# Optimization experiments

Hardware: AMD Instinct MI355X
Metric: run time of the kernel (lower is better)

## Reference

```python
import jax, jax.numpy as jnp
import numpy as np

D_MODEL = 1024
D_STATE = 64
B = 8
L = 8192
REAL_INIT = -0.5
SCALING = 1.0


def _hippo_frequencies(d_state):
    # eigenvalues of (Hippo - Hippo.T)/2, largest imag part first
    N = 2 * d_state
    i = np.arange(N, dtype=np.float64)
    x = 2 * i + 1
    Hippo = np.tril(np.sqrt(np.outer(x, x)), k=-1)
    Skew = (Hippo - Hippo.T) / 2
    evals = np.linalg.eigvals(Skew)
    order = np.argsort(-evals.imag)
    return evals[order][:d_state].imag.astype(np.float32)


def setup_inputs() -> dict:
    key = jax.random.key(0)
    k1, k2, k3, k4 = jax.random.split(key, 4)
    frequencies = jnp.asarray(_hippo_frequencies(D_STATE) * SCALING)
    decays = jnp.full((D_STATE,), np.float32(np.log(abs(REAL_INIT) * SCALING + 1e-10)))
    return {
        "input": jax.random.normal(k1, (B, L, D_MODEL), dtype=jnp.float32),
        "initial_state": jax.random.normal(k2, (B, D_STATE), dtype=jnp.float32),
        "in_projection": jax.random.normal(k3, (D_MODEL, D_STATE), dtype=jnp.float32),
        "out_projection": jax.random.normal(k4, (D_STATE, D_MODEL), dtype=jnp.float32),
        "frequencies": frequencies,
        "decays": decays,
    }


def reference(input, initial_state, in_projection, out_projection, frequencies, decays):
    Bsz, Lseq, H = input.shape
    # project into state space: [B, L, N]
    u = jnp.einsum("blh,hn->bln", input, in_projection)
    # prepend initial state: [B, L+1, N]
    u = jnp.concatenate((initial_state[:, None, :].astype(u.dtype), u), axis=1)
    kernel_len = Lseq + 1
    fft_len = 2 * kernel_len - 1
    # diagonal SSM kernel: exp(t * (-exp(decay) + i*freq)), t = 0..L  -> [kernel_len, N]
    lam = (-jnp.exp(decays) + 1j * frequencies).astype(jnp.complex64)  # [N]
    t = jnp.arange(kernel_len, dtype=jnp.float32)[:, None]  # [kernel_len, 1]
    kernel = jnp.exp(t * lam[None, :])
    # FFT convolution along sequence axis
    u_f = jnp.fft.fft(u, n=fft_len, axis=-2)
    k_f = jnp.fft.fft(kernel, n=fft_len, axis=-2)
    conv = jnp.fft.ifft(u_f * k_f[None, :, :], axis=-2)[:, 1:Lseq + 1, :]
    final_state = conv[:, -1:, :]  # [B, 1, N] complex
    output = jnp.einsum("bln,nh->blh", conv.real, out_projection)
    return output, final_state
```

## Files before the change

kernel.cpp:

```cpp
#include <hip/hip_runtime.h>
#include <math.h>

#define Bz   8
#define Lz   8192
#define Hz   1024
#define Nz   64
#define BLz  (Bz * Lz)

typedef __attribute__((ext_vector_type(8))) short bf16x8;
typedef __attribute__((ext_vector_type(4))) float f32x4;

__device__ inline unsigned int bfpack2(float a, float b) {
    unsigned int ua = __float_as_uint(a) + 0x8000u;
    unsigned int ub = __float_as_uint(b) + 0x8000u;
    return (ua >> 16) | (ub & 0xFFFF0000u);
}
__device__ inline unsigned short bf1(float a) {
    return (unsigned short)((__float_as_uint(a) + 0x8000u) >> 16);
}

__global__ __launch_bounds__(256) void prep_kernel(
    const float* __restrict__ Win, const float* __restrict__ Wout,
    unsigned short* __restrict__ WinT, unsigned short* __restrict__ WoutT)
{
    int i = blockIdx.x * 256 + threadIdx.x;
    if (i < 65536) {
        int n = i >> 10, k = i & 1023;
        WinT[i] = bf1(Win[k * Nz + n]);
    } else {
        int j = i - 65536;
        int h = j >> 6, n = j & 63;
        WoutT[j] = bf1(Wout[n * Hz + h]);
    }
}

__global__ __launch_bounds__(256) void gemm_in_kernel(
    const float* __restrict__ inp, const unsigned short* __restrict__ WinT,
    float* __restrict__ u)
{
    __shared__ unsigned short sA[128][72];
    __shared__ unsigned short sB[64][72];

    const int t    = threadIdx.x;
    const int wid  = t >> 6;
    const int lane = t & 63;
    const int nl   = lane & 15;
    const int q    = lane >> 4;
    const size_t rowBase = (size_t)blockIdx.x * 128;

    f32x4 acc[2][4];
#pragma unroll
    for (int m = 0; m < 2; ++m)
#pragma unroll
        for (int nt = 0; nt < 4; ++nt) acc[m][nt] = (f32x4){0.f, 0.f, 0.f, 0.f};

    for (int kc = 0; kc < Hz; kc += 64) {
        __syncthreads();
#pragma unroll
        for (int j = 0; j < 4; ++j) {
            int f = j * 256 + t;
            int r = f >> 3, c = f & 7;
            const float* p = inp + (rowBase + r) * Hz + kc + c * 8;
            float4 v0 = *reinterpret_cast<const float4*>(p);
            float4 v1 = *reinterpret_cast<const float4*>(p + 4);
            uint4 d;
            d.x = bfpack2(v0.x, v0.y);
            d.y = bfpack2(v0.z, v0.w);
            d.z = bfpack2(v1.x, v1.y);
            d.w = bfpack2(v1.z, v1.w);
            *reinterpret_cast<uint4*>(&sA[r][c * 8]) = d;
        }
#pragma unroll
        for (int j = 0; j < 2; ++j) {
            int f = j * 256 + t;
            int r = f >> 3, c = f & 7;
            uint4 w = *reinterpret_cast<const uint4*>(WinT + (size_t)r * Hz + kc + c * 8);
            *reinterpret_cast<uint4*>(&sB[r][c * 8]) = w;
        }
        __syncthreads();

#pragma unroll
        for (int ks = 0; ks < 2; ++ks) {
            bf16x8 a0 = *reinterpret_cast<bf16x8*>(&sA[wid * 32 + nl][ks * 32 + q * 8]);
            bf16x8 a1 = *reinterpret_cast<bf16x8*>(&sA[wid * 32 + 16 + nl][ks * 32 + q * 8]);
#pragma unroll
            for (int nt = 0; nt < 4; ++nt) {
                bf16x8 b = *reinterpret_cast<bf16x8*>(&sB[nt * 16 + nl][ks * 32 + q * 8]);
                acc[0][nt] = __builtin_amdgcn_mfma_f32_16x16x32_bf16(a0, b, acc[0][nt], 0, 0, 0);
                acc[1][nt] = __builtin_amdgcn_mfma_f32_16x16x32_bf16(a1, b, acc[1][nt], 0, 0, 0);
            }
        }
    }

    const int bI = (int)(rowBase >> 13);
    const int l0 = ((int)rowBase & (Lz - 1)) + wid * 32 + q * 4;
#pragma unroll
    for (int m = 0; m < 2; ++m)
#pragma unroll
        for (int nt = 0; nt < 4; ++nt) {
            const int nn = nt * 16 + nl;
            *reinterpret_cast<f32x4*>(
                u + (((size_t)(bI * Nz + nn)) << 13) + (l0 + m * 16)) = acc[m][nt];
        }
}

#define CHUNK 512
#define WARM  192
#define GSTEP 64

#define SSTEP(UV, IDX)                                              \
    {                                                               \
        float nr_ = fmaf(ar, xr, fmaf(-ai, xi, (UV)));              \
        float ni_ = fmaf(ar, xi, ai * xr);                          \
        xr = nr_; xi = ni_;                                         \
        if (emit_) cp_[(size_t)(IDX) * Nz] = bf1(xr);               \
    }

#define DO_GROUP(BUF, G)                                            \
    {                                                               \
        const int g_ = (G);                                         \
        const bool emit_ = (g_ >= emitG);                           \
        const bool pf_ = (g_ + 2 < nG);                             \
        unsigned short* cp_ = cb + (size_t)(g_ * GSTEP) * Nz;       \
        const float4* np_ = up + (g_ + 2) * (GSTEP / 4);            \
        _Pragma("unroll")                                           \
        for (int k = 0; k < 16; ++k) {                              \
            float4 v_ = BUF[k];                                     \
            if (pf_) BUF[k] = np_[k];                               \
            SSTEP(v_.x, k * 4 + 0)                                  \
            SSTEP(v_.y, k * 4 + 1)                                  \
            SSTEP(v_.z, k * 4 + 2)                                  \
            SSTEP(v_.w, k * 4 + 3)                                  \
        }                                                           \
    }

__global__ __launch_bounds__(64) void scan_kernel(
    const float* __restrict__ ut, const float* __restrict__ init,
    const float* __restrict__ freq, const float* __restrict__ dec,
    unsigned short* __restrict__ convb, float* __restrict__ fs, int fs_mode)
{
    const int n = threadIdx.x;
    const int b = blockIdx.x;
    const int c = blockIdx.y;

    const float mag = expf(-expf(dec[n]));
    const float fr  = freq[n];
    const float ar  = mag * cosf(fr);
    const float ai  = mag * sinf(fr);

    const int s0    = (c == 0) ? 0 : (c * CHUNK - WARM);
    const int nG    = (c == 0) ? (CHUNK / GSTEP) : ((CHUNK + WARM) / GSTEP);
    const int emitG = (c == 0) ? 0 : (WARM / GSTEP);

    const float4* up = reinterpret_cast<const float4*>(
                           ut + (((size_t)(b * Nz + n)) << 13)) + (s0 >> 2);
    unsigned short* cb = convb + ((size_t)b * Lz + s0) * Nz + n;

    float xr = (c == 0) ? init[b * Nz + n] : 0.f;
    float xi = 0.f;

    float4 bufA[16], bufB[16];
#pragma unroll
    for (int k = 0; k < 16; ++k) bufA[k] = up[k];
#pragma unroll
    for (int k = 0; k < 16; ++k) bufB[k] = up[16 + k];

    const int nG2 = nG & ~1;
    for (int g = 0; g < nG2; g += 2) {
        DO_GROUP(bufA, g)
        DO_GROUP(bufB, g + 1)
    }
    if (nG & 1) { DO_GROUP(bufA, nG - 1) }

    if (c == (Lz / CHUNK) - 1 && fs_mode) {
        if (fs_mode == 2) {
            fs[(b * Nz + n) * 2 + 0] = xr;
            fs[(b * Nz + n) * 2 + 1] = xi;
        } else {
            fs[b * Nz + n] = xr;
        }
    }
}

__global__ __launch_bounds__(512) void gemm_out_kernel(
    const unsigned short* __restrict__ convb,
    const unsigned short* __restrict__ WoutT,
    float* __restrict__ out)
{
    __shared__ unsigned short sW[256][72];

    const int t    = threadIdx.x;
    const int wid  = t >> 6;
    const int lane = t & 63;
    const int nl   = lane & 15;
    const int q    = lane >> 4;
    const int hBase = blockIdx.x * 256;
    const size_t rowBase = (size_t)blockIdx.y * 128 + wid * 16;

#pragma unroll
    for (int j = 0; j < 4; ++j) {
        int f = j * 512 + t;
        int r = f >> 3, c = f & 7;
        uint4 v = *reinterpret_cast<const uint4*>(WoutT + (size_t)(hBase + r) * Nz + c * 8);
        *reinterpret_cast<uint4*>(&sW[r][c * 8]) = v;
    }
    __syncthreads();

    const unsigned short* ap = convb + (rowBase + nl) * Nz;
    bf16x8 a0 = *reinterpret_cast<const bf16x8*>(ap + q * 8);
    bf16x8 a1 = *reinterpret_cast<const bf16x8*>(ap + 32 + q * 8);

    const f32x4 zero = (f32x4){0.f, 0.f, 0.f, 0.f};
#pragma unroll
    for (int ht = 0; ht < 16; ++ht) {
        bf16x8 b0 = *reinterpret_cast<bf16x8*>(&sW[ht * 16 + nl][q * 8]);
        bf16x8 b1 = *reinterpret_cast<bf16x8*>(&sW[ht * 16 + nl][32 + q * 8]);
        f32x4 acc = __builtin_amdgcn_mfma_f32_16x16x32_bf16(a0, b0, zero, 0, 0, 0);
        acc = __builtin_amdgcn_mfma_f32_16x16x32_bf16(a1, b1, acc, 0, 0, 0);
#pragma unroll
        for (int reg = 0; reg < 4; ++reg)
            out[(rowBase + q * 4 + reg) * Hz + hBase + ht * 16 + nl] = acc[reg];
    }
}

extern "C" void kernel_launch(void* const* d_in, const int* in_sizes, int n_in,
                              void* d_out, int out_size, void* d_ws, size_t ws_size,
                              hipStream_t stream)
{
    const float* inp  = (const float*)d_in[0];
    const float* init = (const float*)d_in[1];
    const float* Win  = (const float*)d_in[2];
    const float* Wout = (const float*)d_in[3];
    const float* freq = (const float*)d_in[4];
    const float* dec  = (const float*)d_in[5];
    float* out = (float*)d_out;

    char* ws = (char*)d_ws;
    float*          u     = (float*)ws;
    unsigned short* convb = (unsigned short*)(ws + (size_t)BLz * Nz * 4);
    unsigned short* WinT  = (unsigned short*)(ws + (size_t)BLz * Nz * 6);
    unsigned short* WoutT = WinT + (size_t)Nz * Hz;

    const int extra   = out_size - BLz * Hz;
    const int fs_mode = (extra >= 2 * Bz * Nz) ? 2 : (extra >= Bz * Nz ? 1 : 0);
    float* fs = out + (size_t)BLz * Hz;

    hipLaunchKernelGGL(prep_kernel, dim3(512), dim3(256), 0, stream,
                       Win, Wout, WinT, WoutT);
    hipLaunchKernelGGL(gemm_in_kernel, dim3(BLz / 128), dim3(256), 0, stream,
                       inp, WinT, u);
    hipLaunchKernelGGL(scan_kernel, dim3(Bz, Lz / CHUNK), dim3(64), 0, stream,
                       u, init, freq, dec, convb, fs, fs_mode);
    hipLaunchKernelGGL(gemm_out_kernel, dim3(Hz / 256, BLz / 128), dim3(512), 0, stream,
                       convb, WoutT, out);
}
```

Baseline: 512.9 us.

## Load GEMM operands straight to registers with double buffering; transpose output MFMA for vector stores

The input-projection GEMM drops its shared-memory staging and syncthreads. Each single-wave block now loads fp32 activations and bf16 weights directly into registers, converting them in flight, with a two-stage register double buffer across K chunks. The output GEMM swaps the MFMA operand order so each lane holds contiguous output columns and writes them as float4 vector stores instead of scalar strided stores. The trade-off is higher register pressure and redundant weight loads from global/L2 in every block, in exchange for less LDS traffic and barrier overhead.

```diff
diff --git a/kernel.cpp b/kernel.cpp
--- a/kernel.cpp
+++ b/kernel.cpp
@@ -17,6 +17,14 @@
 }
 __device__ inline unsigned short bf1(float a) {
     return (unsigned short)((__float_as_uint(a) + 0x8000u) >> 16);
+}
+__device__ inline bf16x8 packa(float4 v0, float4 v1) {
+    union { uint4 u; bf16x8 h; } cv;
+    cv.u.x = bfpack2(v0.x, v0.y);
+    cv.u.y = bfpack2(v0.z, v0.w);
+    cv.u.z = bfpack2(v1.x, v1.y);
+    cv.u.w = bfpack2(v1.z, v1.w);
+    return cv.h;
 }
 
 __global__ __launch_bounds__(256) void prep_kernel(
@@ -34,19 +42,62 @@
     }
 }
 
-__global__ __launch_bounds__(256) void gemm_in_kernel(
+#define LOADKC(AB, BB, OFF)                                                  \
+    if ((OFF) < Hz) {                                                        \
+        const float* ap0_ = a0p + (OFF);                                     \
+        const float* ap1_ = a1p + (OFF);                                     \
+        AB[0] = *reinterpret_cast<const float4*>(ap0_);                      \
+        AB[1] = *reinterpret_cast<const float4*>(ap0_ + 4);                  \
+        AB[2] = *reinterpret_cast<const float4*>(ap0_ + 32);                 \
+        AB[3] = *reinterpret_cast<const float4*>(ap0_ + 36);                 \
+        AB[4] = *reinterpret_cast<const float4*>(ap1_);                      \
+        AB[5] = *reinterpret_cast<const float4*>(ap1_ + 4);                  \
+        AB[6] = *reinterpret_cast<const float4*>(ap1_ + 32);                 \
+        AB[7] = *reinterpret_cast<const float4*>(ap1_ + 36);                 \
+        BB[0] = *reinterpret_cast<const bf16x8*>(b0p + (OFF));               \
+        BB[1] = *reinterpret_cast<const bf16x8*>(b0p + (OFF) + 32);          \
+        BB[2] = *reinterpret_cast<const bf16x8*>(b1p + (OFF));               \
+        BB[3] = *reinterpret_cast<const bf16x8*>(b1p + (OFF) + 32);          \
+        BB[4] = *reinterpret_cast<const bf16x8*>(b2p + (OFF));               \
+        BB[5] = *reinterpret_cast<const bf16x8*>(b2p + (OFF) + 32);          \
+        BB[6] = *reinterpret_cast<const bf16x8*>(b3p + (OFF));               \
+        BB[7] = *reinterpret_cast<const bf16x8*>(b3p + (OFF) + 32);          \
+    }
+
+#define CONSKC(AB, BB)                                                       \
+    {                                                                        \
+        bf16x8 a00 = packa(AB[0], AB[1]);                                    \
+        bf16x8 a01 = packa(AB[2], AB[3]);                                    \
+        bf16x8 a10 = packa(AB[4], AB[5]);                                    \
+        bf16x8 a11 = packa(AB[6], AB[7]);                                    \
+        _Pragma("unroll")                                                    \
+        for (int nt = 0; nt < 4; ++nt) {                                     \
+            acc[0][nt] = __builtin_amdgcn_mfma_f32_16x16x32_bf16(            \
+                a00, BB[nt * 2 + 0], acc[0][nt], 0, 0, 0);                   \
+            acc[0][nt] = __builtin_amdgcn_mfma_f32_16x16x32_bf16(            \
+                a01, BB[nt * 2 + 1], acc[0][nt], 0, 0, 0);                   \
+            acc[1][nt] = __builtin_amdgcn_mfma_f32_16x16x32_bf16(            \
+                a10, BB[nt * 2 + 0], acc[1][nt], 0, 0, 0);                   \
+            acc[1][nt] = __builtin_amdgcn_mfma_f32_16x16x32_bf16(            \
+                a11, BB[nt * 2 + 1], acc[1][nt], 0, 0, 0);                   \
+        }                                                                    \
+    }
+
+__global__ __launch_bounds__(64) void gemm_in_kernel(
     const float* __restrict__ inp, const unsigned short* __restrict__ WinT,
     float* __restrict__ u)
 {
-    __shared__ unsigned short sA[128][72];
-    __shared__ unsigned short sB[64][72];
-
-    const int t    = threadIdx.x;
-    const int wid  = t >> 6;
-    const int lane = t & 63;
+    const int lane = threadIdx.x;
     const int nl   = lane & 15;
     const int q    = lane >> 4;
-    const size_t rowBase = (size_t)blockIdx.x * 128;
+    const size_t rowBase = (size_t)blockIdx.x * 32;
+
+    const float* a0p = inp + (rowBase + nl) * Hz + q * 8;
+    const float* a1p = inp + (rowBase + 16 + nl) * Hz + q * 8;
+    const unsigned short* b0p = WinT + (size_t)(0 * 16 + nl) * Hz + q * 8;
+    const unsigned short* b1p = WinT + (size_t)(1 * 16 + nl) * Hz + q * 8;
+    const unsigned short* b2p = WinT + (size_t)(2 * 16 + nl) * Hz + q * 8;
+    const unsigned short* b3p = WinT + (size_t)(3 * 16 + nl) * Hz + q * 8;
 
     f32x4 acc[2][4];
 #pragma unroll
@@ -54,46 +105,21 @@
 #pragma unroll
         for (int nt = 0; nt < 4; ++nt) acc[m][nt] = (f32x4){0.f, 0.f, 0.f, 0.f};
 
-    for (int kc = 0; kc < Hz; kc += 64) {
-        __syncthreads();
-#pragma unroll
-        for (int j = 0; j < 4; ++j) {
-            int f = j * 256 + t;
-            int r = f >> 3, c = f & 7;
-            const float* p = inp + (rowBase + r) * Hz + kc + c * 8;
-            float4 v0 = *reinterpret_cast<const float4*>(p);
-            float4 v1 = *reinterpret_cast<const float4*>(p + 4);
-            uint4 d;
-            d.x = bfpack2(v0.x, v0.y);
-            d.y = bfpack2(v0.z, v0.w);
-            d.z = bfpack2(v1.x, v1.y);
-            d.w = bfpack2(v1.z, v1.w);
-            *reinterpret_cast<uint4*>(&sA[r][c * 8]) = d;
-        }
-#pragma unroll
-        for (int j = 0; j < 2; ++j) {
-            int f = j * 256 + t;
-            int r = f >> 3, c = f & 7;
-            uint4 w = *reinterpret_cast<const uint4*>(WinT + (size_t)r * Hz + kc + c * 8);
-            *reinterpret_cast<uint4*>(&sB[r][c * 8]) = w;
-        }
-        __syncthreads();
-
-#pragma unroll
-        for (int ks = 0; ks < 2; ++ks) {
-            bf16x8 a0 = *reinterpret_cast<bf16x8*>(&sA[wid * 32 + nl][ks * 32 + q * 8]);
-            bf16x8 a1 = *reinterpret_cast<bf16x8*>(&sA[wid * 32 + 16 + nl][ks * 32 + q * 8]);
-#pragma unroll
-            for (int nt = 0; nt < 4; ++nt) {
-                bf16x8 b = *reinterpret_cast<bf16x8*>(&sB[nt * 16 + nl][ks * 32 + q * 8]);
-                acc[0][nt] = __builtin_amdgcn_mfma_f32_16x16x32_bf16(a0, b, acc[0][nt], 0, 0, 0);
-                acc[1][nt] = __builtin_amdgcn_mfma_f32_16x16x32_bf16(a1, b, acc[1][nt], 0, 0, 0);
-            }
-        }
+    float4 A0[8], A1[8];
+    bf16x8 B0[8], B1[8];
+    LOADKC(A0, B0, 0)
+    LOADKC(A1, B1, 64)
+
+#pragma unroll
+    for (int g = 0; g < 8; ++g) {
+        CONSKC(A0, B0)
+        LOADKC(A0, B0, g * 128 + 128)
+        CONSKC(A1, B1)
+        LOADKC(A1, B1, g * 128 + 192)
     }
 
     const int bI = (int)(rowBase >> 13);
-    const int l0 = ((int)rowBase & (Lz - 1)) + wid * 32 + q * 4;
+    const int l0 = ((int)rowBase & (Lz - 1)) + q * 4;
 #pragma unroll
     for (int m = 0; m < 2; ++m)
 #pragma unroll
@@ -195,7 +221,7 @@
     const int nl   = lane & 15;
     const int q    = lane >> 4;
     const int hBase = blockIdx.x * 256;
-    const size_t rowBase = (size_t)blockIdx.y * 128 + wid * 16;
+    const size_t blBase = (size_t)blockIdx.y * 128 + wid * 16;
 
 #pragma unroll
     for (int j = 0; j < 4; ++j) {
@@ -204,22 +230,21 @@
         uint4 v = *reinterpret_cast<const uint4*>(WoutT + (size_t)(hBase + r) * Nz + c * 8);
         *reinterpret_cast<uint4*>(&sW[r][c * 8]) = v;
     }
+
+    const unsigned short* bp = convb + (blBase + nl) * Nz + q * 8;
+    bf16x8 b0 = *reinterpret_cast<const bf16x8*>(bp);
+    bf16x8 b1 = *reinterpret_cast<const bf16x8*>(bp + 32);
     __syncthreads();
 
-    const unsigned short* ap = convb + (rowBase + nl) * Nz;
-    bf16x8 a0 = *reinterpret_cast<const bf16x8*>(ap + q * 8);
-    bf16x8 a1 = *reinterpret_cast<const bf16x8*>(ap + 32 + q * 8);
-
+    float* op = out + (blBase + nl) * Hz + hBase + q * 4;
     const f32x4 zero = (f32x4){0.f, 0.f, 0.f, 0.f};
 #pragma unroll
     for (int ht = 0; ht < 16; ++ht) {
-        bf16x8 b0 = *reinterpret_cast<bf16x8*>(&sW[ht * 16 + nl][q * 8]);
-        bf16x8 b1 = *reinterpret_cast<bf16x8*>(&sW[ht * 16 + nl][32 + q * 8]);
-        f32x4 acc = __builtin_amdgcn_mfma_f32_16x16x32_bf16(a0, b0, zero, 0, 0, 0);
-        acc = __builtin_amdgcn_mfma_f32_16x16x32_bf16(a1, b1, acc, 0, 0, 0);
-#pragma unroll
-        for (int reg = 0; reg < 4; ++reg)
-            out[(rowBase + q * 4 + reg) * Hz + hBase + ht * 16 + nl] = acc[reg];
+        bf16x8 w0 = *reinterpret_cast<bf16x8*>(&sW[ht * 16 + nl][q * 8]);
+        bf16x8 w1 = *reinterpret_cast<bf16x8*>(&sW[ht * 16 + nl][32 + q * 8]);
+        f32x4 acc = __builtin_amdgcn_mfma_f32_16x16x32_bf16(w0, b0, zero, 0, 0, 0);
+        acc = __builtin_amdgcn_mfma_f32_16x16x32_bf16(w1, b1, acc, 0, 0, 0);
+        *reinterpret_cast<f32x4*>(op + ht * 16) = acc;
     }
 }
 
@@ -247,7 +272,7 @@
 
     hipLaunchKernelGGL(prep_kernel, dim3(512), dim3(256), 0, stream,
                        Win, Wout, WinT, WoutT);
-    hipLaunchKernelGGL(gemm_in_kernel, dim3(BLz / 128), dim3(256), 0, stream,
+    hipLaunchKernelGGL(gemm_in_kernel, dim3(BLz / 32), dim3(64), 0, stream,
                        inp, WinT, u);
     hipLaunchKernelGGL(scan_kernel, dim3(Bz, Lz / CHUNK), dim3(64), 0, stream,
                        u, init, freq, dec, convb, fs, fs_mode);
```

Result: slower. 535.7 us (+4.5%).
